# Performance work log

Hardware: AMD Instinct MI355X
Metric: run time of the kernel (lower is better)

## Reference

```python
import jax, jax.numpy as jnp
import numpy as np

N_HEADS = 12

def setup_inputs() -> dict:
    key = jax.random.key(0)
    k1, k2, k3 = jax.random.split(key, 3)
    B, N, D = 2, 2048, 768
    x = jax.random.normal(k1, (B, N, D), dtype=jnp.float32)
    # Linear weights stored as [in, out] (equivalent to torch W.T)
    Wkqv = jax.random.normal(k2, (D, 3 * D), dtype=jnp.float32) * (1.0 / np.sqrt(D))
    bkqv = jnp.zeros((3 * D,), dtype=jnp.float32)
    Wproj = jax.random.normal(k3, (D, D), dtype=jnp.float32) * (1.0 / np.sqrt(D))
    bproj = jnp.zeros((D,), dtype=jnp.float32)
    return {"x": x, "Wkqv": Wkqv, "bkqv": bkqv, "Wproj": Wproj, "bproj": bproj}


def reference(x, Wkqv, bkqv, Wproj, bproj):
    B, N, D = x.shape
    H = N_HEADS
    hd = D // H
    kqv = x @ Wkqv + bkqv                     # [B, N, 3D]
    # NOTE: original chunks in (k, q, v) order
    k, q, v = jnp.split(kqv, 3, axis=-1)
    k = k.reshape(B, N, H, hd).transpose(0, 2, 1, 3)   # [B, H, N, hd]
    q = q.reshape(B, N, H, hd).transpose(0, 2, 1, 3)
    v = v.reshape(B, N, H, hd).transpose(0, 2, 1, 3)
    att = jnp.einsum('bhqd,bhkd->bhqk', q, k) / jnp.sqrt(jnp.float32(hd))
    causal = jnp.tril(jnp.ones((N, N), dtype=bool))    # [N, N]
    att = jnp.where(causal[None, None, :, :], att, jnp.float32(-jnp.inf))
    w = jax.nn.softmax(att, axis=-1)
    sa = jnp.einsum('bhqk,bhkd->bhqd', w, v)           # [B, H, N, hd]
    sa = sa.transpose(0, 2, 1, 3).reshape(B, N, D)
    return sa @ Wproj + bproj
```

## Files before the change

kernel.cpp:

```cpp
#include <hip/hip_runtime.h>

typedef __attribute__((ext_vector_type(8))) short bf16x8;
typedef __attribute__((ext_vector_type(4))) float f32x4;
typedef __attribute__((ext_vector_type(16))) float f32x16;

#define BATCH 2
#define SEQ 2048
#define DMODEL 768
#define NH 12
#define HD 64
#define M_TOK (BATCH * SEQ)
#define N_KQV (3 * DMODEL)

#define GLOAD16(gsrc, ldst) __builtin_amdgcn_global_load_lds( \
    (const __attribute__((address_space(1))) unsigned int*)(const void*)(gsrc), \
    (__attribute__((address_space(3))) unsigned int*)(void*)(ldst), 16, 0, 0)

__device__ __forceinline__ unsigned short f2bf(float f) {
  unsigned int u = __float_as_uint(f);
  u += 0x7FFFu + ((u >> 16) & 1u);
  return (unsigned short)(u >> 16);
}

__device__ __forceinline__ unsigned int cvtpk(float lo, float hi) {
  unsigned int r;
  asm("v_cvt_pk_bf16_f32 %0, %1, %2" : "=v"(r) : "v"(lo), "v"(hi));
  return r;
}


__global__ void cvt_f32_bf16(const float* __restrict__ in,
                             unsigned short* __restrict__ out, int n4) {
  int i = blockIdx.x * blockDim.x + threadIdx.x;
  if (i >= n4) return;
  float4 v = reinterpret_cast<const float4*>(in)[i];
  unsigned long long p = (unsigned long long)f2bf(v.x)
                       | ((unsigned long long)f2bf(v.y) << 16)
                       | ((unsigned long long)f2bf(v.z) << 32)
                       | ((unsigned long long)f2bf(v.w) << 48);
  reinterpret_cast<unsigned long long*>(out)[i] = p;
}

__global__ void transpose_cvt(const float* __restrict__ in,
                              unsigned short* __restrict__ out,
                              int rows, int cols) {
  __shared__ float tile[32][33];
  int c0 = blockIdx.x * 32, r0 = blockIdx.y * 32;
  for (int i = threadIdx.y; i < 32; i += 8)
    tile[i][threadIdx.x] = in[(size_t)(r0 + i) * cols + c0 + threadIdx.x];
  __syncthreads();
  for (int i = threadIdx.y; i < 32; i += 8)
    out[(size_t)(c0 + i) * rows + r0 + threadIdx.x] = f2bf(tile[threadIdx.x][i]);
}

template <int BM, int BN, int MODE>
__global__ __launch_bounds__(256) void gemm_bt(
    const unsigned short* __restrict__ A,
    const unsigned short* __restrict__ BT,
    const float* __restrict__ bias,
    int M, int N, int K,
    unsigned short* __restrict__ outK, unsigned short* __restrict__ outQ,
    unsigned short* __restrict__ outVT, float* __restrict__ outF) {
  constexpr int WTN = BN / 2;
  constexpr int NACC = WTN / 32;
  constexpr int L = BM / 64 + BN / 64;
  __shared__ __align__(16) unsigned short lds_a[2][BM][32];
  __shared__ __align__(16) unsigned short lds_b[2][BN][32];
  const int tid = threadIdx.x;
  const int lane = tid & 63;
  const int w = tid >> 6;
  const int wm = w >> 1, wn = w & 1;
  const int l31 = lane & 31, hi = lane >> 5;
  const int m0 = blockIdx.y * BM, n0 = blockIdx.x * BN;

  f32x16 acc[NACC];
#pragma unroll
  for (int j = 0; j < NACC; j++)
#pragma unroll
    for (int i = 0; i < 16; i++) acc[j][i] = 0.f;

  const int srow = lane >> 2;
  const int sg = ((lane & 3) ^ ((lane >> 3) & 3)) * 8;
  const int xq = (l31 >> 1) & 3;

#define STAGE(buf, k0)                                                        \
  {                                                                           \
    _Pragma("unroll")                                                         \
    for (int rr = 0; rr < BM / 64; ++rr)                                      \
      GLOAD16(&A[(size_t)(m0 + rr * 64 + w * 16 + srow) * K + (k0) + sg],     \
              &lds_a[buf][rr * 64 + w * 16][0]);                              \
    _Pragma("unroll")                                                         \
    for (int rr = 0; rr < BN / 64; ++rr)                                      \
      GLOAD16(&BT[(size_t)(n0 + rr * 64 + w * 16 + srow) * K + (k0) + sg],    \
              &lds_b[buf][rr * 64 + w * 16][0]);                              \
  }

  const int KT = K >> 5;
  STAGE(0, 0);
  STAGE(1, 32);

  for (int kt = 0; kt < KT; ++kt) {
    const int cur = kt & 1;
    if (kt + 1 < KT) {
      if constexpr (L == 3) asm volatile("s_waitcnt vmcnt(3)" ::: "memory");
      else                  asm volatile("s_waitcnt vmcnt(2)" ::: "memory");
    } else {
      asm volatile("s_waitcnt vmcnt(0)" ::: "memory");
    }
    __builtin_amdgcn_s_barrier();
    __builtin_amdgcn_sched_barrier(0);

    bf16x8 aA[2], aB[2][NACC];
#pragma unroll
    for (int ds = 0; ds < 2; ds++) {
      const int rc = ((ds * 2 + hi) ^ xq) * 8;
      aA[ds] = *(const bf16x8*)&lds_a[cur][wm * 32 + l31][rc];
#pragma unroll
      for (int j = 0; j < NACC; j++)
        aB[ds][j] = *(const bf16x8*)&lds_b[cur][wn * WTN + j * 32 + l31][rc];
    }
#pragma unroll
    for (int ds = 0; ds < 2; ds++)
#pragma unroll
      for (int j = 0; j < NACC; j++)
        acc[j] = __builtin_amdgcn_mfma_f32_32x32x16_bf16(aA[ds], aB[ds][j], acc[j], 0, 0, 0);

    __builtin_amdgcn_s_barrier();
    if (kt + 2 < KT) STAGE(cur, (kt + 2) << 5);
  }
#undef STAGE

#pragma unroll
  for (int j = 0; j < NACC; j++) {
#pragma unroll
    for (int r = 0; r < 16; r++) {
      int row = m0 + wm * 32 + (r & 3) + 8 * (r >> 2) + 4 * hi;
      int col = n0 + wn * WTN + j * 32 + l31;
      float v = acc[j][r] + bias[col];
      if (MODE == 0) {
        int chunk = col / DMODEL;
        int d = col - chunk * DMODEL;
        int hh = d >> 6, di = d & 63;
        int bb = row >> 11, tok = row & 2047;
        int bh = bb * NH + hh;
        if (chunk == 0)
          outK[((size_t)bh * SEQ + tok) * HD + di] = f2bf(v);
        else if (chunk == 1)
          outQ[((size_t)bh * SEQ + tok) * HD + di] = f2bf(v * 0.125f);
        else
          outVT[((size_t)bh * HD + di) * SEQ + tok] = f2bf(v);
      } else {
        outF[(size_t)row * N + col] = v;
      }
    }
  }
}

__global__ __launch_bounds__(128) void attn_kernel(
    const unsigned short* __restrict__ qbuf,
    const unsigned short* __restrict__ kbuf,
    const unsigned short* __restrict__ vT,
    unsigned short* __restrict__ sa) {
  __shared__ __align__(16) char smem_raw[18432];
  auto k_lds = reinterpret_cast<unsigned short (*)[72]>(smem_raw);
  auto v_lds = reinterpret_cast<unsigned short (*)[72]>(smem_raw + 9216);
  auto o_merge = reinterpret_cast<float (*)[32][33]>(smem_raw);
  auto l_merge = reinterpret_cast<float (*)[32]>(smem_raw + 9216);

  const int tid = threadIdx.x, lane = tid & 63, w = tid >> 6;
  const int l31 = lane & 31, hi = lane >> 5;

  const int fid = (int)blockIdx.y * (int)gridDim.x + (int)blockIdx.x;
  const int xcd = fid & 7, slot = fid >> 3;
  const int bh = ((slot >> 6) << 3) + xcd;
  const int t = 63 - (slot & 63);
  const int ktmax = t >> 1;

  const size_t qk_base = (size_t)bh * SEQ * HD;
  const size_t v_base = (size_t)bh * HD * SEQ;
  const int bb = bh / NH, h = bh - bb * NH;

  const int sr = w * 32 + (lane >> 3);
  const int sc = (lane & 7) * 8;

  {
    bf16x8 rk[4], rv[4];
#pragma unroll
    for (int p = 0; p < 4; p++) {
      rk[p] = *(const bf16x8*)&kbuf[qk_base + (size_t)(sr + 8 * p) * HD + sc];
      rv[p] = *(const bf16x8*)&vT[v_base + (size_t)(sr + 8 * p) * SEQ + sc];
    }
#pragma unroll
    for (int p = 0; p < 4; p++) {
      *(bf16x8*)&k_lds[sr + 8 * p][sc] = rk[p];
      *(bf16x8*)&v_lds[sr + 8 * p][sc] = rv[p];
    }
  }

  bf16x8 aq[4];
#pragma unroll
  for (int ds = 0; ds < 4; ds++)
    aq[ds] = *(const bf16x8*)&qbuf[qk_base + (size_t)(t * 32 + l31) * HD + ds * 16 + hi * 8];

  f32x16 o0, o1;
#pragma unroll
  for (int i = 0; i < 16; i++) { o0[i] = 0.f; o1[i] = 0.f; }
  float lsum = 0.f;

  __syncthreads();

  for (int kt = 0; kt <= ktmax; ++kt) {
    const bool more = (kt < ktmax);
    bf16x8 rk[4], rv[4];
    if (more) {
      const int nrow = (kt + 1) * 64;
#pragma unroll
      for (int p = 0; p < 4; p++) {
        rk[p] = *(const bf16x8*)&kbuf[qk_base + (size_t)(nrow + sr + 8 * p) * HD + sc];
        rv[p] = *(const bf16x8*)&vT[v_base + (size_t)(sr + 8 * p) * SEQ + nrow + sc];
      }
    }

    f32x16 s;
#pragma unroll
    for (int i = 0; i < 16; i++) s[i] = 0.f;
    __builtin_amdgcn_s_setprio(1);
#pragma unroll
    for (int ds = 0; ds < 4; ds++) {
      bf16x8 bk = *(const bf16x8*)&k_lds[w * 32 + l31][ds * 16 + hi * 8];
      s = __builtin_amdgcn_mfma_f32_32x32x16_bf16(bk, aq[ds], s, 0, 0, 0);
    }
    __builtin_amdgcn_s_setprio(0);

    const bool diag = (kt == ktmax);
    const int qb2 = (t & 1) * 32;
#pragma unroll
    for (int r = 0; r < 16; r++) {
      int kr = (r & 3) + 8 * (r >> 2) + 4 * hi;
      float val = s[r];
      if (diag && (w * 32 + kr > qb2 + l31)) val = -1e30f;
      float p = __expf(val);
      s[r] = p;
      lsum += p;
    }

    union { unsigned int u[4]; bf16x8 v; } f1, f2;
    {
      unsigned int A = cvtpk(s[0], s[1]), B = cvtpk(s[2], s[3]);
      unsigned int C = cvtpk(s[4], s[5]), D = cvtpk(s[6], s[7]);
      auto rAC = __builtin_amdgcn_permlane32_swap(A, C, false, false);
      auto rBD = __builtin_amdgcn_permlane32_swap(B, D, false, false);
      f1.u[0] = rAC[0]; f1.u[1] = rBD[0]; f1.u[2] = rAC[1]; f1.u[3] = rBD[1];
      unsigned int A2 = cvtpk(s[8], s[9]),   B2 = cvtpk(s[10], s[11]);
      unsigned int C2 = cvtpk(s[12], s[13]), D2 = cvtpk(s[14], s[15]);
      auto rAC2 = __builtin_amdgcn_permlane32_swap(A2, C2, false, false);
      auto rBD2 = __builtin_amdgcn_permlane32_swap(B2, D2, false, false);
      f2.u[0] = rAC2[0]; f2.u[1] = rBD2[0]; f2.u[2] = rAC2[1]; f2.u[3] = rBD2[1];
    }

    __builtin_amdgcn_s_setprio(1);
    {
      bf16x8 bv00 = *(const bf16x8*)&v_lds[l31][w * 32 + hi * 8];
      bf16x8 bv01 = *(const bf16x8*)&v_lds[32 + l31][w * 32 + hi * 8];
      o0 = __builtin_amdgcn_mfma_f32_32x32x16_bf16(f1.v, bv00, o0, 0, 0, 0);
      o1 = __builtin_amdgcn_mfma_f32_32x32x16_bf16(f1.v, bv01, o1, 0, 0, 0);
      bf16x8 bv10 = *(const bf16x8*)&v_lds[l31][w * 32 + 16 + hi * 8];
      bf16x8 bv11 = *(const bf16x8*)&v_lds[32 + l31][w * 32 + 16 + hi * 8];
      o0 = __builtin_amdgcn_mfma_f32_32x32x16_bf16(f2.v, bv10, o0, 0, 0, 0);
      o1 = __builtin_amdgcn_mfma_f32_32x32x16_bf16(f2.v, bv11, o1, 0, 0, 0);
    }
    __builtin_amdgcn_s_setprio(0);

    if (more) {
      __syncthreads();
#pragma unroll
      for (int p = 0; p < 4; p++) {
        *(bf16x8*)&k_lds[sr + 8 * p][sc] = rk[p];
        *(bf16x8*)&v_lds[sr + 8 * p][sc] = rv[p];
      }
      __syncthreads();
    }
  }

  __syncthreads();
  {
    float ltot = lsum + __shfl_xor(lsum, 32);
    if (hi == 0) l_merge[w][l31] = ltot;
    f32x16 osend = w ? o0 : o1;
#pragma unroll
    for (int r = 0; r < 16; r++) {
      int ql = (r & 3) + 8 * (r >> 2) + 4 * hi;
      o_merge[w][ql][l31] = osend[r];
    }
    __syncthreads();
    f32x16 okeep = w ? o1 : o0;
#pragma unroll
    for (int r = 0; r < 16; r++) {
      int ql = (r & 3) + 8 * (r >> 2) + 4 * hi;
      float ot = okeep[r] + o_merge[1 - w][ql][l31];
      float lt = l_merge[0][ql] + l_merge[1][ql];
      sa[((size_t)bb * SEQ + t * 32 + ql) * DMODEL + h * HD + w * 32 + l31] = f2bf(ot / lt);
    }
  }
}


extern "C" void kernel_launch(void* const* d_in, const int* in_sizes, int n_in,
                              void* d_out, int out_size, void* d_ws, size_t ws_size,
                              hipStream_t stream) {
  const float* x     = (const float*)d_in[0];
  const float* Wkqv  = (const float*)d_in[1];
  const float* bkqv  = (const float*)d_in[2];
  const float* Wproj = (const float*)d_in[3];
  const float* bproj = (const float*)d_in[4];
  float* out = (float*)d_out;

  char* ws = (char*)d_ws;
  unsigned short* x_bf   = (unsigned short*)(ws + 0);
  unsigned short* wkqvT  = (unsigned short*)(ws + 6291456);
  unsigned short* wprojT = (unsigned short*)(ws + 9830400);
  unsigned short* qb     = (unsigned short*)(ws + 11010048);
  unsigned short* kb     = (unsigned short*)(ws + 17301504);
  unsigned short* vT     = (unsigned short*)(ws + 23592960);
  unsigned short* sa     = (unsigned short*)(ws + 29884416);

  cvt_f32_bf16<<<(M_TOK * DMODEL / 4 + 255) / 256, 256, 0, stream>>>(x, x_bf, M_TOK * DMODEL / 4);
  transpose_cvt<<<dim3(N_KQV / 32, DMODEL / 32), dim3(32, 8), 0, stream>>>(Wkqv, wkqvT, DMODEL, N_KQV);
  transpose_cvt<<<dim3(DMODEL / 32, DMODEL / 32), dim3(32, 8), 0, stream>>>(Wproj, wprojT, DMODEL, DMODEL);

  gemm_bt<64, 128, 0><<<dim3(N_KQV / 128, M_TOK / 64), 256, 0, stream>>>(
      x_bf, wkqvT, bkqv, M_TOK, N_KQV, DMODEL, kb, qb, vT, nullptr);

  attn_kernel<<<dim3(64, BATCH * NH), 128, 0, stream>>>(qb, kb, vT, sa);

  gemm_bt<64, 64, 1><<<dim3(DMODEL / 64, M_TOK / 64), 256, 0, stream>>>(
      sa, wprojT, bproj, M_TOK, DMODEL, DMODEL, nullptr, nullptr, nullptr, out);
}
```

Baseline: 111.7 us.

## Use 128x128 tiles with 2x2 MFMA per wave in KQV GEMM; reorder attention blocks

The GEMM template now gives each wave an MI x NJ grid of 32x32 accumulators, and the KQV projection moves from 64x128 to 128x128 tiles. Each LDS-loaded A/B fragment therefore feeds more MFMAs, raising data reuse, at the cost of more accumulator registers and half as many blocks. The attention grid mapping also changes so that consecutive slots cycle through three heads per XCD while walking query tiles from heaviest to lightest, which interleaves causal workloads across heads for better load balance.

```diff
diff --git a/kernel.cpp b/kernel.cpp
--- a/kernel.cpp
+++ b/kernel.cpp
@@ -61,8 +61,8 @@
     int M, int N, int K,
     unsigned short* __restrict__ outK, unsigned short* __restrict__ outQ,
     unsigned short* __restrict__ outVT, float* __restrict__ outF) {
-  constexpr int WTN = BN / 2;
-  constexpr int NACC = WTN / 32;
+  constexpr int MI = BM / 64;
+  constexpr int NJ = BN / 64;
   constexpr int L = BM / 64 + BN / 64;
   __shared__ __align__(16) unsigned short lds_a[2][BM][32];
   __shared__ __align__(16) unsigned short lds_b[2][BN][32];
@@ -73,11 +73,13 @@
   const int l31 = lane & 31, hi = lane >> 5;
   const int m0 = blockIdx.y * BM, n0 = blockIdx.x * BN;
 
-  f32x16 acc[NACC];
-#pragma unroll
-  for (int j = 0; j < NACC; j++)
-#pragma unroll
-    for (int i = 0; i < 16; i++) acc[j][i] = 0.f;
+  f32x16 acc[MI][NJ];
+#pragma unroll
+  for (int mi = 0; mi < MI; mi++)
+#pragma unroll
+    for (int nj = 0; nj < NJ; nj++)
+#pragma unroll
+      for (int i = 0; i < 16; i++) acc[mi][nj][i] = 0.f;
 
   const int srow = lane >> 2;
   const int sg = ((lane & 3) ^ ((lane >> 3) & 3)) * 8;
@@ -102,28 +104,34 @@
   for (int kt = 0; kt < KT; ++kt) {
     const int cur = kt & 1;
     if (kt + 1 < KT) {
-      if constexpr (L == 3) asm volatile("s_waitcnt vmcnt(3)" ::: "memory");
-      else                  asm volatile("s_waitcnt vmcnt(2)" ::: "memory");
+      if constexpr (L == 4)      asm volatile("s_waitcnt vmcnt(4)" ::: "memory");
+      else if constexpr (L == 3) asm volatile("s_waitcnt vmcnt(3)" ::: "memory");
+      else                       asm volatile("s_waitcnt vmcnt(2)" ::: "memory");
     } else {
       asm volatile("s_waitcnt vmcnt(0)" ::: "memory");
     }
     __builtin_amdgcn_s_barrier();
     __builtin_amdgcn_sched_barrier(0);
 
-    bf16x8 aA[2], aB[2][NACC];
+    bf16x8 aA[2][MI], aB[2][NJ];
 #pragma unroll
     for (int ds = 0; ds < 2; ds++) {
       const int rc = ((ds * 2 + hi) ^ xq) * 8;
-      aA[ds] = *(const bf16x8*)&lds_a[cur][wm * 32 + l31][rc];
-#pragma unroll
-      for (int j = 0; j < NACC; j++)
-        aB[ds][j] = *(const bf16x8*)&lds_b[cur][wn * WTN + j * 32 + l31][rc];
+#pragma unroll
+      for (int mi = 0; mi < MI; mi++)
+        aA[ds][mi] = *(const bf16x8*)&lds_a[cur][wm * (BM / 2) + mi * 32 + l31][rc];
+#pragma unroll
+      for (int nj = 0; nj < NJ; nj++)
+        aB[ds][nj] = *(const bf16x8*)&lds_b[cur][wn * (BN / 2) + nj * 32 + l31][rc];
     }
 #pragma unroll
     for (int ds = 0; ds < 2; ds++)
 #pragma unroll
-      for (int j = 0; j < NACC; j++)
-        acc[j] = __builtin_amdgcn_mfma_f32_32x32x16_bf16(aA[ds], aB[ds][j], acc[j], 0, 0, 0);
+      for (int mi = 0; mi < MI; mi++)
+#pragma unroll
+        for (int nj = 0; nj < NJ; nj++)
+          acc[mi][nj] = __builtin_amdgcn_mfma_f32_32x32x16_bf16(
+              aA[ds][mi], aB[ds][nj], acc[mi][nj], 0, 0, 0);
 
     __builtin_amdgcn_s_barrier();
     if (kt + 2 < KT) STAGE(cur, (kt + 2) << 5);
@@ -131,26 +139,29 @@
 #undef STAGE
 
 #pragma unroll
-  for (int j = 0; j < NACC; j++) {
-#pragma unroll
-    for (int r = 0; r < 16; r++) {
-      int row = m0 + wm * 32 + (r & 3) + 8 * (r >> 2) + 4 * hi;
-      int col = n0 + wn * WTN + j * 32 + l31;
-      float v = acc[j][r] + bias[col];
-      if (MODE == 0) {
-        int chunk = col / DMODEL;
-        int d = col - chunk * DMODEL;
-        int hh = d >> 6, di = d & 63;
-        int bb = row >> 11, tok = row & 2047;
-        int bh = bb * NH + hh;
-        if (chunk == 0)
-          outK[((size_t)bh * SEQ + tok) * HD + di] = f2bf(v);
-        else if (chunk == 1)
-          outQ[((size_t)bh * SEQ + tok) * HD + di] = f2bf(v * 0.125f);
-        else
-          outVT[((size_t)bh * HD + di) * SEQ + tok] = f2bf(v);
-      } else {
-        outF[(size_t)row * N + col] = v;
+  for (int mi = 0; mi < MI; mi++) {
+#pragma unroll
+    for (int nj = 0; nj < NJ; nj++) {
+#pragma unroll
+      for (int r = 0; r < 16; r++) {
+        int row = m0 + wm * (BM / 2) + mi * 32 + (r & 3) + 8 * (r >> 2) + 4 * hi;
+        int col = n0 + wn * (BN / 2) + nj * 32 + l31;
+        float v = acc[mi][nj][r] + bias[col];
+        if (MODE == 0) {
+          int chunk = col / DMODEL;
+          int d = col - chunk * DMODEL;
+          int hh = d >> 6, di = d & 63;
+          int bb = row >> 11, tok = row & 2047;
+          int bh = bb * NH + hh;
+          if (chunk == 0)
+            outK[((size_t)bh * SEQ + tok) * HD + di] = f2bf(v);
+          else if (chunk == 1)
+            outQ[((size_t)bh * SEQ + tok) * HD + di] = f2bf(v * 0.125f);
+          else
+            outVT[((size_t)bh * HD + di) * SEQ + tok] = f2bf(v);
+        } else {
+          outF[(size_t)row * N + col] = v;
+        }
       }
     }
   }
@@ -172,8 +183,9 @@
 
   const int fid = (int)blockIdx.y * (int)gridDim.x + (int)blockIdx.x;
   const int xcd = fid & 7, slot = fid >> 3;
-  const int bh = ((slot >> 6) << 3) + xcd;
-  const int t = 63 - (slot & 63);
+  const int head3 = slot % 3;
+  const int t = 63 - slot / 3;
+  const int bh = head3 * 8 + xcd;
   const int ktmax = t >> 1;
 
   const size_t qk_base = (size_t)bh * SEQ * HD;
@@ -328,7 +340,7 @@
   transpose_cvt<<<dim3(N_KQV / 32, DMODEL / 32), dim3(32, 8), 0, stream>>>(Wkqv, wkqvT, DMODEL, N_KQV);
   transpose_cvt<<<dim3(DMODEL / 32, DMODEL / 32), dim3(32, 8), 0, stream>>>(Wproj, wprojT, DMODEL, DMODEL);
 
-  gemm_bt<64, 128, 0><<<dim3(N_KQV / 128, M_TOK / 64), 256, 0, stream>>>(
+  gemm_bt<128, 128, 0><<<dim3(N_KQV / 128, M_TOK / 128), 256, 0, stream>>>(
       x_bf, wkqvT, bkqv, M_TOK, N_KQV, DMODEL, kb, qb, vT, nullptr);
 
   attn_kernel<<<dim3(64, BATCH * NH), 128, 0, stream>>>(qb, kb, vT, sa);
```

Result: faster. 107.9 us (-3.4%).
